# Performance work log

Hardware: AMD Instinct MI355X
Metric: run time of the kernel (lower is better)

Reference implementation:

```python
import jax, jax.numpy as jnp
import numpy as np

SIGMA_MAX = 25.0

def marginal_prob_std(t):
    # VE-SDE std: sqrt((sigma_max^(2t) - 1) / (2 ln sigma_max))
    log_s = jnp.log(SIGMA_MAX)
    return jnp.sqrt((jnp.exp(2.0 * t * log_s) - 1.0) / (2.0 * log_s))

def setup_inputs() -> dict:
    key = jax.random.key(0)
    k1, k2, k3 = jax.random.split(key, 3)
    B, N, d = 16384, 16384, 1
    x = jax.random.normal(k1, (B, d), dtype=jnp.float32)
    t = jax.random.uniform(k2, (B,), dtype=jnp.float32, minval=1e-3, maxval=1.0)
    train_data = jax.random.normal(k3, (N, d), dtype=jnp.float32)
    return {"x": x, "t": t, "train_data": train_data}

def reference(x, t, train_data):
    # x: [B,1], t: [B], train_data: [N,1]
    sigma = marginal_prob_std(t)                       # [B]
    sigma2 = sigma * sigma                             # [B]
    # pairwise squared distance (d=1): [N, B]
    diff = train_data - x[:, 0][None, :]               # [N,1]-[1,B] -> broadcast fails; do explicit
    diff = train_data[:, 0][:, None] - x[:, 0][None, :]  # [N, B]
    pdf = jnp.exp(-0.5 * (diff * diff) / sigma2[None, :])  # [N, B]
    num = jnp.sum(pdf * train_data, axis=0)            # [N,B]*[N,1] -> [B]
    den = jnp.sum(pdf, axis=0)                         # [B]
    den_safe = jnp.where(den == 0.0, 1.0, den)
    evals = jnp.where(den == 0.0, 0.0, num / den_safe) # nan -> 0 as in torch code
    evals = evals[:, None]                             # [B,1]
    return (evals - x) / sigma2[:, None]
```

## Files before the change

kernel.cpp:

```cpp
#include <hip/hip_runtime.h>
#include <math.h>


typedef float v2f __attribute__((ext_vector_type(2)));

#define BLK   256
#define JB    16
#define PARTS 16
#define CH    2048

#if __has_builtin(__builtin_amdgcn_exp2f)
#define EXP2(x) __builtin_amdgcn_exp2f(x)
#else
#define EXP2(x) exp2f(x)
#endif

__device__ __forceinline__ float sigma2_of(float tj) {
  const float TWO_LOG_S = 6.4377516497364011f;
  return (__expf(TWO_LOG_S * tj) - 1.0f) / TWO_LOG_S;
}

__device__ __forceinline__ float4 load_pad(const float* __restrict__ td,
                                           int gi, int N) {
  if (gi + 3 < N) return *(const float4*)(td + gi);
  float4 v;
  v.x = (gi + 0 < N) ? td[gi + 0] : 1e30f;
  v.y = (gi + 1 < N) ? td[gi + 1] : 1e30f;
  v.z = (gi + 2 < N) ? td[gi + 2] : 1e30f;
  v.w = (gi + 3 < N) ? td[gi + 3] : 1e30f;
  return v;
}

__launch_bounds__(BLK, 4)
__global__ void gmm_fused(const float* __restrict__ x,
                          const float* __restrict__ t,
                          const float* __restrict__ td,
                          float* __restrict__ out,
                          int N, int B) {
  __shared__ float lds[CH];
  __shared__ float nbuf[PARTS * JB];
  __shared__ float dbuf[PARTS * JB];

  const int tid  = threadIdx.x;
  const int jl   = tid & (JB - 1);
  const int part = tid >> 4;
  const int j    = blockIdx.x * JB + jl;

  float r = 0.0f, y = 0.0f;
  if (j < B) {
    const float HALF_LOG2E = 0.72134752044448170f;
    float s2 = sigma2_of(t[j]);
    r = __fsqrt_rn(HALF_LOG2E / s2);
    y = x[j] * r;
  }

  const v2f rv  = {r, r};
  const v2f nyv = {-y, -y};

  v2f n0 = {0.f, 0.f}, n1 = {0.f, 0.f}, n2 = {0.f, 0.f}, n3 = {0.f, 0.f};
  v2f d0 = {0.f, 0.f}, d1 = {0.f, 0.f}, d2 = {0.f, 0.f}, d3 = {0.f, 0.f};

#define GROUP(v, nacc, dacc)                                            \
  {                                                                     \
    v2f dd = __builtin_elementwise_fma(v, rv, nyv);                     \
    v2f qq = dd * dd;                                                   \
    v2f pp;                                                             \
    pp.x = EXP2(-qq.x); pp.y = EXP2(-qq.y);                             \
    dacc += pp;                                                         \
    nacc = __builtin_elementwise_fma(pp, v, nacc);                      \
  }

  const int NC = (N + CH - 1) / CH;
  const float4* l4 = (const float4*)lds;

  float4 pA = load_pad(td, tid * 4, N);
  float4 pB = load_pad(td, (tid + BLK) * 4, N);

  for (int c = 0; c < NC; ++c) {
    float4 nA = pA, nB = pB;
    if (c + 1 < NC) {
      const int nb = (c + 1) * CH;
      nA = load_pad(td, nb + tid * 4, N);
      nB = load_pad(td, nb + (tid + BLK) * 4, N);
    }

    ((float4*)lds)[tid]       = pA;
    ((float4*)lds)[tid + BLK] = pB;
    __syncthreads();

    #pragma unroll 4
    for (int k = 0; k < CH / 64; k += 2) {
      float4 v0 = l4[part + 16 * k];
      float4 v1 = l4[part + 16 * k + 16];
      v2f va = {v0.x, v0.y}, vb = {v0.z, v0.w};
      v2f vc = {v1.x, v1.y}, vd = {v1.z, v1.w};
      GROUP(va, n0, d0)
      GROUP(vb, n1, d1)
      GROUP(vc, n2, d2)
      GROUP(vd, n3, d3)
    }
    __syncthreads();

    pA = nA;
    pB = nB;
  }
#undef GROUP

  v2f numv = (n0 + n1) + (n2 + n3);
  v2f denv = (d0 + d1) + (d2 + d3);
  nbuf[part * JB + jl] = numv.x + numv.y;
  dbuf[part * JB + jl] = denv.x + denv.y;
  __syncthreads();

  if (tid < JB && (blockIdx.x * JB + tid) < B) {
    const int jj = blockIdx.x * JB + tid;
    float num = 0.f, den = 0.f;
    #pragma unroll
    for (int p = 0; p < PARTS; ++p) {
      num += nbuf[p * JB + tid];
      den += dbuf[p * JB + tid];
    }
    float sigma2 = sigma2_of(t[jj]);
    float evals = (den == 0.0f) ? 0.0f : (num / den);
    out[jj] = (evals - x[jj]) / sigma2;
  }
}

extern "C" void kernel_launch(void* const* d_in, const int* in_sizes, int n_in,
                              void* d_out, int out_size, void* d_ws, size_t ws_size,
                              hipStream_t stream) {
  const float* x  = (const float*)d_in[0];
  const float* t  = (const float*)d_in[1];
  const float* td = (const float*)d_in[2];
  float* out = (float*)d_out;
  (void)d_ws; (void)ws_size;

  const int B = in_sizes[0];
  const int N = in_sizes[2];

  const int GX = (B + JB - 1) / JB;
  gmm_fused<<<GX, BLK, 0, stream>>>(x, t, td, out, N, B);
}
```

Before: 92.38 us.

## Double-buffer LDS chunks and double chunk size to halve barriers

Switches the shared-memory staging of training data to two ping-pong buffers, so each chunk needs one barrier instead of two. The chunk size also goes from 2048 to 4096 elements, halving the number of chunk iterations. The cost is 32KB of LDS per block instead of 8KB and four outstanding float4 prefetch registers per thread, which may lower occupancy from the 4 blocks per CU set in the launch bounds.

```diff
diff --git a/kernel.cpp b/kernel.cpp
--- a/kernel.cpp
+++ b/kernel.cpp
@@ -7,7 +7,7 @@
 #define BLK   256
 #define JB    16
 #define PARTS 16
-#define CH    2048
+#define CH    4096
 
 #if __has_builtin(__builtin_amdgcn_exp2f)
 #define EXP2(x) __builtin_amdgcn_exp2f(x)
@@ -37,7 +37,7 @@
                           const float* __restrict__ td,
                           float* __restrict__ out,
                           int N, int B) {
-  __shared__ float lds[CH];
+  __shared__ float lds[2][CH];
   __shared__ float nbuf[PARTS * JB];
   __shared__ float dbuf[PARTS * JB];
 
@@ -71,23 +71,32 @@
   }
 
   const int NC = (N + CH - 1) / CH;
-  const float4* l4 = (const float4*)lds;
 
-  float4 pA = load_pad(td, tid * 4, N);
-  float4 pB = load_pad(td, (tid + BLK) * 4, N);
+  {
+    float4 s0 = load_pad(td, (tid          ) * 4, N);
+    float4 s1 = load_pad(td, (tid +     BLK) * 4, N);
+    float4 s2 = load_pad(td, (tid + 2 * BLK) * 4, N);
+    float4 s3 = load_pad(td, (tid + 3 * BLK) * 4, N);
+    float4* dst = (float4*)lds[0];
+    dst[tid]           = s0;
+    dst[tid +     BLK] = s1;
+    dst[tid + 2 * BLK] = s2;
+    dst[tid + 3 * BLK] = s3;
+  }
+  __syncthreads();
 
   for (int c = 0; c < NC; ++c) {
-    float4 nA = pA, nB = pB;
-    if (c + 1 < NC) {
+    float4 s0 = {0,0,0,0}, s1 = {0,0,0,0}, s2 = {0,0,0,0}, s3 = {0,0,0,0};
+    const bool more = (c + 1 < NC);
+    if (more) {
       const int nb = (c + 1) * CH;
-      nA = load_pad(td, nb + tid * 4, N);
-      nB = load_pad(td, nb + (tid + BLK) * 4, N);
+      s0 = load_pad(td, nb + (tid          ) * 4, N);
+      s1 = load_pad(td, nb + (tid +     BLK) * 4, N);
+      s2 = load_pad(td, nb + (tid + 2 * BLK) * 4, N);
+      s3 = load_pad(td, nb + (tid + 3 * BLK) * 4, N);
     }
 
-    ((float4*)lds)[tid]       = pA;
-    ((float4*)lds)[tid + BLK] = pB;
-    __syncthreads();
-
+    const float4* l4 = (const float4*)lds[c & 1];
     #pragma unroll 4
     for (int k = 0; k < CH / 64; k += 2) {
       float4 v0 = l4[part + 16 * k];
@@ -99,15 +108,21 @@
       GROUP(vc, n2, d2)
       GROUP(vd, n3, d3)
     }
-    __syncthreads();
 
-    pA = nA;
-    pB = nB;
+    if (more) {
+      float4* dst = (float4*)lds[(c + 1) & 1];
+      dst[tid]           = s0;
+      dst[tid +     BLK] = s1;
+      dst[tid + 2 * BLK] = s2;
+      dst[tid + 3 * BLK] = s3;
+      __syncthreads();
+    }
   }
 #undef GROUP
 
   v2f numv = (n0 + n1) + (n2 + n3);
   v2f denv = (d0 + d1) + (d2 + d3);
+  __syncthreads();
   nbuf[part * JB + jl] = numv.x + numv.y;
   dbuf[part * JB + jl] = denv.x + denv.y;
   __syncthreads();
```

Measured after the change: 91.95 us, median of 2. No clear change (-0.5%).
